# Kernel optimization log

Measured on AMD Instinct MI355X. Metric: run time of the kernel, lower is better.

## Reference

```python
import jax, jax.numpy as jnp
import numpy as np

N_NODES = 50000
N_EDGES = 800000
NEG_SLOPE = 0.2


def _gat_conv(h, src, dst, W, al, ar, b, res, act):
    """DGL-style GATConv. h:[N,Fin], W:[Fin,H*D], al/ar:[H,D], b:[H*D].
    res: None | [N,H,D] residual value. Returns [N,H,D]."""
    N = h.shape[0]
    H, D = al.shape
    ft = (h @ W).reshape(N, H, D)                       # projected features
    el = jnp.einsum('nhd,hd->nh', ft, al)               # [N,H]
    er = jnp.einsum('nhd,hd->nh', ft, ar)               # [N,H]
    e = jax.nn.leaky_relu(el[src] + er[dst], NEG_SLOPE) # [E,H] edge logits
    # edge softmax over incoming edges of each dst node
    emax = jax.ops.segment_max(e, dst, num_segments=N)  # [N,H]
    emax = jnp.where(jnp.isfinite(emax), emax, 0.0)     # guard empty segments
    ex = jnp.exp(e - emax[dst])                         # [E,H]
    denom = jax.ops.segment_sum(ex, dst, num_segments=N)
    a = ex / denom[dst]                                 # [E,H] attention
    rst = jax.ops.segment_sum(ft[src] * a[..., None], dst, num_segments=N)  # [N,H,D]
    if res is not None:
        rst = rst + res
    rst = rst + b.reshape(1, H, D)
    if act is not None:
        rst = act(rst)
    return rst


def setup_inputs() -> dict:
    key = jax.random.key(0)
    ks = jax.random.split(key, 16)
    s = 0.1
    return {
        'x': jax.random.normal(ks[0], (N_NODES, 128), jnp.float32),
        'edge_src': jax.random.randint(ks[1], (N_EDGES,), 0, N_NODES, jnp.int32),
        'edge_dst': jax.random.randint(ks[2], (N_EDGES,), 0, N_NODES, jnp.int32),
        'W0': jax.random.normal(ks[3], (128, 128), jnp.float32) * s,
        'al0': jax.random.normal(ks[4], (2, 64), jnp.float32) * s,
        'ar0': jax.random.normal(ks[5], (2, 64), jnp.float32) * s,
        'b0': jnp.zeros((128,), jnp.float32),
        'W1': jax.random.normal(ks[6], (128, 128), jnp.float32) * s,
        'al1': jax.random.normal(ks[7], (2, 64), jnp.float32) * s,
        'ar1': jax.random.normal(ks[8], (2, 64), jnp.float32) * s,
        'b1': jnp.zeros((128,), jnp.float32),
        'W2': jax.random.normal(ks[9], (128, 194), jnp.float32) * s,
        'al2': jax.random.normal(ks[10], (2, 97), jnp.float32) * s,
        'ar2': jax.random.normal(ks[11], (2, 97), jnp.float32) * s,
        'b2': jnp.zeros((194,), jnp.float32),
        'res_W2': jax.random.normal(ks[12], (128, 194), jnp.float32) * s,
    }


def reference(x, edge_src, edge_dst, W0, al0, ar0, b0, W1, al1, ar1, b1,
              W2, al2, ar2, b2, res_W2):
    N = x.shape[0]
    elu = jax.nn.elu
    # layer 0: no residual, ELU
    h = _gat_conv(x, edge_src, edge_dst, W0, al0, ar0, b0, None, elu)
    h = h.reshape(N, -1)                                # flatten(1) -> [N,128]
    # layer 1: identity residual (in == heads*out), ELU
    res1 = h.reshape(N, 2, 64)
    h = _gat_conv(h, edge_src, edge_dst, W1, al1, ar1, b1, res1, elu)
    h = h.reshape(N, -1)
    # output layer: linear residual, no activation, mean over heads
    res2 = (h @ res_W2).reshape(N, 2, 97)
    logits = _gat_conv(h, edge_src, edge_dst, W2, al2, ar2, b2, res2, None)
    logits = logits.mean(axis=1)                        # [N, 97]
    # original slices off the last node of each graph (single batched graph)
    return logits[: N - 1]
```

## Files before the change

kernel.cpp:

```cpp
#include <hip/hip_runtime.h>
#include <math.h>

#define NNODES 50000
#define NEDGES 800000
#define NPAD   50048

typedef unsigned int uint;
typedef unsigned short u16;
typedef __bf16 bf16x8 __attribute__((ext_vector_type(8)));
typedef float f32x4 __attribute__((ext_vector_type(4)));

__device__ __forceinline__ float lrelu(float x){ return x > 0.f ? x : 0.2f*x; }
__device__ __forceinline__ float elu_f(float x){ return x > 0.f ? x : expm1f(x); }
__device__ __forceinline__ u16 f2bf(float f){
    uint u = __float_as_uint(f);
    return (u16)((u + 0x7fffu + ((u >> 16) & 1u)) >> 16);
}
__device__ __forceinline__ float bf2f(u16 h){ return __uint_as_float(((uint)h) << 16); }
__device__ __forceinline__ float blo(uint u){ return __uint_as_float(u << 16); }
__device__ __forceinline__ float bhi(uint u){ return __uint_as_float(u & 0xffff0000u); }

__global__ void split_x(const float* __restrict__ x, u16* __restrict__ Xh, u16* __restrict__ Xl, int N)
{
    int idx = blockIdx.x * blockDim.x + threadIdx.x;
    if (idx >= NPAD * 32) return;
    int n = idx >> 5;
    float4 v = make_float4(0.f, 0.f, 0.f, 0.f);
    if (n < N) v = ((const float4*)x)[idx];
    ushort4 h, l;
    h.x = f2bf(v.x); l.x = f2bf(v.x - bf2f(h.x));
    h.y = f2bf(v.y); l.y = f2bf(v.y - bf2f(h.y));
    h.z = f2bf(v.z); l.z = f2bf(v.z - bf2f(h.z));
    h.w = f2bf(v.w); l.w = f2bf(v.w - bf2f(h.w));
    ((ushort4*)Xh)[idx] = h;
    ((ushort4*)Xl)[idx] = l;
}

__global__ void split_w_hi(const float* __restrict__ W, u16* __restrict__ Bh, int Cc, int CP)
{
    int idx = blockIdx.x * blockDim.x + threadIdx.x;
    if (idx >= CP * 128) return;
    int col = idx >> 7, k = idx & 127;
    float v = (col < Cc) ? W[k * Cc + col] : 0.f;
    Bh[idx] = f2bf(v);
}

__global__ void zero_pad2(u16* __restrict__ Hh, u16* __restrict__ Hl)
{
    int idx = blockIdx.x * blockDim.x + threadIdx.x;
    if (idx < (NPAD - NNODES) * 128) {
        Hh[(size_t)NNODES * 128 + idx] = 0;
        Hl[(size_t)NNODES * 128 + idx] = 0;
    }
}

__global__ __launch_bounds__(256, 4)
void gemm_l01(const u16* __restrict__ Ah, const u16* __restrict__ Al,
              const u16* __restrict__ Bh, u16* __restrict__ obf,
              const float* __restrict__ alv, const float* __restrict__ arv,
              float* __restrict__ el, float* __restrict__ er, int N)
{
    __shared__ u16 sB[128 * 136];
    const int bm = blockIdx.x * 64;
    const int tid = threadIdx.x, wid = tid >> 6, lane = tid & 63;
    const int lr = lane & 15, q = lane >> 4, lk8 = q << 3;

    bf16x8 aH[4], aL[4];
    {
        size_t abase = (size_t)(bm + wid*16 + lr) * 128 + lk8;
        #pragma unroll
        for (int kt = 0; kt < 4; kt++) {
            aH[kt] = *(const bf16x8*)(Ah + abase + kt*32);
            aL[kt] = *(const bf16x8*)(Al + abase + kt*32);
        }
    }
    {
        const int c = tid >> 1, seg = (tid & 1) * 64;
        const u16* g = Bh + (size_t)c * 128 + seg;
        u16* s = sB + c * 136 + seg;
        #pragma unroll
        for (int j = 0; j < 8; j++)
            *(uint4*)(s + j*8) = *(const uint4*)(g + j*8);
    }
    __syncthreads();

    f32x4 acc[8];
    #pragma unroll
    for (int i = 0; i < 8; i++) acc[i] = (f32x4){0.f,0.f,0.f,0.f};

    #pragma unroll
    for (int kt = 0; kt < 4; kt++)
        #pragma unroll
        for (int fs = 0; fs < 8; fs++) {
            bf16x8 b = *(const bf16x8*)(sB + (fs*16 + lr)*136 + kt*32 + lk8);
            acc[fs] = __builtin_amdgcn_mfma_f32_16x16x32_bf16(aH[kt], b, acc[fs], 0, 0, 0);
            acc[fs] = __builtin_amdgcn_mfma_f32_16x16x32_bf16(aL[kt], b, acc[fs], 0, 0, 0);
        }

    float el0[4] = {0,0,0,0}, el1[4] = {0,0,0,0}, er0[4] = {0,0,0,0}, er1[4] = {0,0,0,0};
    #pragma unroll
    for (int fs = 0; fs < 8; fs++) {
        const int col = fs*16 + lr;
        const float av = alv[col], gv = arv[col];
        #pragma unroll
        for (int v = 0; v < 4; v++) {
            float f = acc[fs][v];
            int row = bm + wid*16 + q*4 + v;
            if (row < N) obf[(size_t)row * 128 + col] = f2bf(f);
            if (fs < 4) { el0[v] += f * av; er0[v] += f * gv; }
            else        { el1[v] += f * av; er1[v] += f * gv; }
        }
    }
    #pragma unroll
    for (int off = 1; off < 16; off <<= 1) {
        #pragma unroll
        for (int v = 0; v < 4; v++) {
            el0[v] += __shfl_xor(el0[v], off);
            el1[v] += __shfl_xor(el1[v], off);
            er0[v] += __shfl_xor(er0[v], off);
            er1[v] += __shfl_xor(er1[v], off);
        }
    }
    if (lr == 0) {
        #pragma unroll
        for (int v = 0; v < 4; v++) {
            int row = bm + wid*16 + q*4 + v;
            if (row < N) {
                *(float2*)(el + 2*(size_t)row) = make_float2(el0[v], el1[v]);
                *(float2*)(er + 2*(size_t)row) = make_float2(er0[v], er1[v]);
            }
        }
    }
}

__global__ __launch_bounds__(256, 4)
void gemm_l2(const u16* __restrict__ Ah, const u16* __restrict__ Al,
             const u16* __restrict__ B2, const u16* __restrict__ Br,
             u16* __restrict__ obf, float* __restrict__ of32, int N)
{
    __shared__ u16 sB[128 * 136];
    const int bid = blockIdx.x;
    const int x = (bid >> 5) * 8 + (bid & 7);
    const int sel = (bid >> 3) & 3;
    if (x >= NPAD / 64) return;
    const bool second = (sel >= 2);
    const int coloff = (sel & 1) * 128;
    const u16* __restrict__ B = second ? Br : B2;

    const int bm = x * 64;
    const int tid = threadIdx.x, wid = tid >> 6, lane = tid & 63;
    const int lr = lane & 15, q = lane >> 4, lk8 = q << 3;

    bf16x8 aH[4], aL[4];
    {
        size_t abase = (size_t)(bm + wid*16 + lr) * 128 + lk8;
        #pragma unroll
        for (int kt = 0; kt < 4; kt++) {
            aH[kt] = *(const bf16x8*)(Ah + abase + kt*32);
            aL[kt] = *(const bf16x8*)(Al + abase + kt*32);
        }
    }
    {
        const int c = tid >> 1, seg = (tid & 1) * 64;
        const u16* g = B + (size_t)(coloff + c) * 128 + seg;
        u16* s = sB + c * 136 + seg;
        #pragma unroll
        for (int j = 0; j < 8; j++)
            *(uint4*)(s + j*8) = *(const uint4*)(g + j*8);
    }
    __syncthreads();

    f32x4 acc[8];
    #pragma unroll
    for (int i = 0; i < 8; i++) acc[i] = (f32x4){0.f,0.f,0.f,0.f};

    #pragma unroll
    for (int kt = 0; kt < 4; kt++)
        #pragma unroll
        for (int fs = 0; fs < 8; fs++) {
            bf16x8 b = *(const bf16x8*)(sB + (fs*16 + lr)*136 + kt*32 + lk8);
            acc[fs] = __builtin_amdgcn_mfma_f32_16x16x32_bf16(aH[kt], b, acc[fs], 0, 0, 0);
            acc[fs] = __builtin_amdgcn_mfma_f32_16x16x32_bf16(aL[kt], b, acc[fs], 0, 0, 0);
        }

    #pragma unroll
    for (int fs = 0; fs < 8; fs++) {
        const int col = coloff + fs*16 + lr;
        if (col >= 194) continue;
        #pragma unroll
        for (int v = 0; v < 4; v++) {
            int row = bm + wid*16 + q*4 + v;
            if (row < N) {
                if (second) of32[(size_t)row * 194 + col] = acc[fs][v];
                else        obf[(size_t)row * 194 + col] = f2bf(acc[fs][v]);
            }
        }
    }
}

template<int C, int D>
__global__ void compute_elr(const uint* __restrict__ ftb, const float* __restrict__ al,
                            const float* __restrict__ ar, float* __restrict__ el,
                            float* __restrict__ er, int N)
{
    int wv = threadIdx.x >> 6, lane = threadIdx.x & 63;
    int n = blockIdx.x * 4 + wv;
    if (n >= N) return;
    const uint* row = ftb + (size_t)n * (C/2);
    float l0=0.f, l1=0.f, r0=0.f, r1=0.f;
    for (int p = lane; p < C/2; p += 64) {
        uint u = row[p];
        float f0 = blo(u), f1 = bhi(u);
        int c0 = 2*p, c1 = 2*p + 1;
        float a0 = al[c0], a1 = al[c1], g0 = ar[c0], g1 = ar[c1];
        if (c0 < D) { l0 += f0*a0; r0 += f0*g0; } else { l1 += f0*a0; r1 += f0*g0; }
        if (c1 < D) { l0 += f1*a1; r0 += f1*g1; } else { l1 += f1*a1; r1 += f1*g1; }
    }
    #pragma unroll
    for (int off = 32; off; off >>= 1) {
        l0 += __shfl_down(l0, off); l1 += __shfl_down(l1, off);
        r0 += __shfl_down(r0, off); r1 += __shfl_down(r1, off);
    }
    if (lane == 0) { el[2*n] = l0; el[2*n+1] = l1; er[2*n] = r0; er[2*n+1] = r1; }
}

__global__ void hist_kernel(const int* __restrict__ dst, int* __restrict__ counts, int E)
{
    int i = blockIdx.x * blockDim.x + threadIdx.x;
    if (i < E) atomicAdd(&counts[dst[i]], 1);
}

__global__ __launch_bounds__(1024)
void scan_local(const int* __restrict__ counts, int* __restrict__ row_start,
                int* __restrict__ partials, int n)
{
    __shared__ int wsum[16];
    const int tid = threadIdx.x, lane = tid & 63, wv = tid >> 6;
    const int i0 = blockIdx.x * 4096 + tid * 4;
    int v[4];
    #pragma unroll
    for (int j = 0; j < 4; j++) { int i = i0 + j; v[j] = (i < n) ? counts[i] : 0; }
    v[1] += v[0]; v[2] += v[1]; v[3] += v[2];
    int t = v[3];
    #pragma unroll
    for (int off = 1; off < 64; off <<= 1) {
        int u = __shfl_up(t, off);
        if (lane >= off) t += u;
    }
    int texcl = t - v[3];
    if (lane == 63) wsum[wv] = t;
    __syncthreads();
    int woff = 0;
    for (int w = 0; w < 16; w++) if (w < wv) woff += wsum[w];
    #pragma unroll
    for (int j = 0; j < 4; j++) { int i = i0 + j; if (i < n) row_start[i+1] = woff + texcl + v[j]; }
    if (tid == 0) {
        int tot = 0;
        for (int w = 0; w < 16; w++) tot += wsum[w];
        partials[blockIdx.x] = tot;
    }
}

__global__ void scan_offs(int* __restrict__ partials, int nb)
{
    int lane = threadIdx.x;
    int v = (lane < nb) ? partials[lane] : 0;
    int t = v;
    #pragma unroll
    for (int off = 1; off < 64; off <<= 1) {
        int u = __shfl_up(t, off);
        if (lane >= off) t += u;
    }
    if (lane < nb) partials[lane] = t - v;
}

__global__ __launch_bounds__(1024)
void scan_add(int* __restrict__ row_start, const int* __restrict__ partials, int n)
{
    const int tid = threadIdx.x;
    const int add = partials[blockIdx.x];
    const int i0 = blockIdx.x * 4096 + tid * 4;
    #pragma unroll
    for (int j = 0; j < 4; j++) { int i = i0 + j; if (i < n) row_start[i+1] += add; }
    if (blockIdx.x == 0 && tid == 0) row_start[0] = 0;
}

__global__ void scatter_kernel(const int* __restrict__ src, const int* __restrict__ dst,
                               const int* __restrict__ row_start, int* __restrict__ cursor,
                               int* __restrict__ src_sorted, int E)
{
    int i = blockIdx.x * blockDim.x + threadIdx.x;
    if (i < E) {
        int d = dst[i];
        int p = atomicAdd(&cursor[d], 1);
        src_sorted[row_start[d] + p] = src[i];
    }
}

template<int MODE>
__global__ __launch_bounds__(256)
void gat_agg128(const uint* __restrict__ ftb, const float* __restrict__ el,
                const float* __restrict__ er, const int* __restrict__ row_start,
                const int* __restrict__ ssorted, const u16* __restrict__ Rh,
                const u16* __restrict__ Rl, const float* __restrict__ bias,
                u16* __restrict__ Hh, u16* __restrict__ Hl)
{
    __shared__ int   s_src[4][64];
    __shared__ float s_w[4][2][64];
    const int wv = threadIdx.x >> 6, lane = threadIdx.x & 63;
    const int n = blockIdx.x * 4 + wv;
    const int beg = row_start[n];
    const int deg = row_start[n+1] - beg;
    const float2 ern = *(const float2*)(er + 2*(size_t)n);
    const int h = lane >> 5;
    float ax = 0.f, ay = 0.f, dp0 = 0.f, dp1 = 0.f;

    for (int cb = 0; cb < deg; cb += 64) {
        const int cnt = min(64, deg - cb);
        float w0 = 0.f, w1 = 0.f; int s = 0;
        if (lane < cnt) {
            s = ssorted[beg + cb + lane];
            float2 e = *(const float2*)(el + 2*(size_t)s);
            w0 = __expf(lrelu(e.x + ern.x));
            w1 = __expf(lrelu(e.y + ern.y));
        }
        dp0 += w0; dp1 += w1;
        s_src[wv][lane] = s; s_w[wv][0][lane] = w0; s_w[wv][1][lane] = w1;
        asm volatile("s_waitcnt lgkmcnt(0)" ::: "memory");
        int t = 0;
        for (; t + 4 <= cnt; t += 4) {
            int4   s4 = *(const int4*)&s_src[wv][t];
            float4 w4 = *(const float4*)&s_w[wv][h][t];
            uint u0 = ftb[((uint)s4.x << 6) + lane];
            uint u1 = ftb[((uint)s4.y << 6) + lane];
            uint u2 = ftb[((uint)s4.z << 6) + lane];
            uint u3 = ftb[((uint)s4.w << 6) + lane];
            ax += w4.x*blo(u0); ay += w4.x*bhi(u0);
            ax += w4.y*blo(u1); ay += w4.y*bhi(u1);
            ax += w4.z*blo(u2); ay += w4.z*bhi(u2);
            ax += w4.w*blo(u3); ay += w4.w*bhi(u3);
        }
        for (; t < cnt; t++) {
            int sv = s_src[wv][t];
            float w = s_w[wv][h][t];
            uint u = ftb[((uint)sv << 6) + lane];
            ax += w*blo(u); ay += w*bhi(u);
        }
    }
    #pragma unroll
    for (int off = 32; off; off >>= 1) { dp0 += __shfl_xor(dp0, off); dp1 += __shfl_xor(dp1, off); }
    const float den = (h == 0) ? dp0 : dp1;
    float r0 = (deg > 0) ? ax / den : 0.f;
    float r1 = (deg > 0) ? ay / den : 0.f;
    const int c0 = 2 * lane;
    const size_t ob = (size_t)n*128 + c0;
    const float2 bv = *(const float2*)(bias + c0);
    float v0 = r0 + bv.x, v1 = r1 + bv.y;
    if (MODE == 1) {
        ushort2 rh = *(const ushort2*)&Rh[ob];
        ushort2 rl = *(const ushort2*)&Rl[ob];
        v0 += bf2f(rh.x) + bf2f(rl.x);
        v1 += bf2f(rh.y) + bf2f(rl.y);
    }
    v0 = elu_f(v0); v1 = elu_f(v1);
    u16 h0 = f2bf(v0), h1v = f2bf(v1);
    *(ushort2*)&Hh[ob] = make_ushort2(h0, h1v);
    *(ushort2*)&Hl[ob] = make_ushort2(f2bf(v0 - bf2f(h0)), f2bf(v1 - bf2f(h1v)));
}

__global__ __launch_bounds__(256)
void gat_agg_out(const uint* __restrict__ ftb, const float* __restrict__ el,
                 const float* __restrict__ er, const int* __restrict__ row_start,
                 const int* __restrict__ ssorted, const float* __restrict__ res,
                 const float* __restrict__ bias, float* __restrict__ out)
{
    __shared__ int   s_src[4][64];
    __shared__ float s_w[4][2][64];
    __shared__ float s_a1[4][97];
    const int wv = threadIdx.x >> 6, lane = threadIdx.x & 63;
    const int n = blockIdx.x * 4 + wv;
    if (n >= NNODES - 1) return;
    const int beg = row_start[n];
    const int deg = row_start[n+1] - beg;
    const float2 ern = *(const float2*)(er + 2*(size_t)n);
    const bool dual = (lane < 33);
    const bool xh0 = (lane <= 48), yh0 = (lane <= 47);
    float ax1=0.f, ay1=0.f, ax2=0.f, ay2=0.f, dp0=0.f, dp1=0.f;

    for (int cb = 0; cb < deg; cb += 64) {
        const int cnt = min(64, deg - cb);
        float w0 = 0.f, w1 = 0.f; int s = 0;
        if (lane < cnt) {
            s = ssorted[beg + cb + lane];
            float2 e = *(const float2*)(el + 2*(size_t)s);
            w0 = __expf(lrelu(e.x + ern.x));
            w1 = __expf(lrelu(e.y + ern.y));
        }
        dp0 += w0; dp1 += w1;
        s_src[wv][lane] = s; s_w[wv][0][lane] = w0; s_w[wv][1][lane] = w1;
        asm volatile("s_waitcnt lgkmcnt(0)" ::: "memory");
        int t = 0;
        for (; t + 4 <= cnt; t += 4) {
            int4   s4 = *(const int4*)&s_src[wv][t];
            float4 q0 = *(const float4*)&s_w[wv][0][t];
            float4 q1 = *(const float4*)&s_w[wv][1][t];
            #pragma unroll
            for (int j = 0; j < 4; j++) {
                int sv = (j==0) ? s4.x : (j==1) ? s4.y : (j==2) ? s4.z : s4.w;
                float f0 = (j==0) ? q0.x : (j==1) ? q0.y : (j==2) ? q0.z : q0.w;
                float f1 = (j==0) ? q1.x : (j==1) ? q1.y : (j==2) ? q1.z : q1.w;
                const uint* row = ftb + (uint)sv * 97u;
                uint u1 = row[lane];
                uint u2 = dual ? row[64 + lane] : 0u;
                float wx = xh0 ? f0 : f1, wy = yh0 ? f0 : f1;
                ax1 += wx*blo(u1); ay1 += wy*bhi(u1);
                ax2 += f1*blo(u2); ay2 += f1*bhi(u2);
            }
        }
        for (; t < cnt; t++) {
            int sv = s_src[wv][t];
            float f0 = s_w[wv][0][t], f1 = s_w[wv][1][t];
            const uint* row = ftb + (uint)sv * 97u;
            uint u1 = row[lane];
            uint u2 = dual ? row[64 + lane] : 0u;
            float wx = xh0 ? f0 : f1, wy = yh0 ? f0 : f1;
            ax1 += wx*blo(u1); ay1 += wy*bhi(u1);
            ax2 += f1*blo(u2); ay2 += f1*bhi(u2);
        }
    }
    #pragma unroll
    for (int off = 32; off; off >>= 1) { dp0 += __shfl_xor(dp0, off); dp1 += __shfl_xor(dp1, off); }
    const float i0 = (deg > 0) ? 1.f/dp0 : 0.f;
    const float i1 = (deg > 0) ? 1.f/dp1 : 0.f;
    float A0x = ax1 * (xh0 ? i0 : i1);
    float A0y = ay1 * (yh0 ? i0 : i1);
    float A2x = ax2 * i1, A2y = ay2 * i1;
    if (lane == 48)      s_a1[wv][0] = A0y;
    else if (lane >= 49) { s_a1[wv][2*lane - 97] = A0x; s_a1[wv][2*lane - 96] = A0y; }
    if (dual)            { s_a1[wv][31 + 2*lane] = A2x; s_a1[wv][32 + 2*lane] = A2y; }
    asm volatile("s_waitcnt lgkmcnt(0)" ::: "memory");
    if (lane <= 48) {
        const int c = 2 * lane;
        const float* rr = res + (size_t)n * 194;
        out[(size_t)n*97 + c] = 0.5f*(A0x + s_a1[wv][c] + rr[c] + rr[97+c] + bias[c] + bias[97+c]);
        if (lane < 48)
            out[(size_t)n*97 + c + 1] = 0.5f*(A0y + s_a1[wv][c+1] + rr[c+1] + rr[98+c] + bias[c+1] + bias[98+c]);
    }
}

extern "C" void kernel_launch(void* const* d_in, const int* in_sizes, int n_in,
                              void* d_out, int out_size, void* d_ws, size_t ws_size,
                              hipStream_t stream)
{
    const float* x   = (const float*)d_in[0];
    const int*   esrc= (const int*)  d_in[1];
    const int*   edst= (const int*)  d_in[2];
    const float* W0  = (const float*)d_in[3];
    const float* al0 = (const float*)d_in[4];
    const float* ar0 = (const float*)d_in[5];
    const float* b0  = (const float*)d_in[6];
    const float* W1  = (const float*)d_in[7];
    const float* al1 = (const float*)d_in[8];
    const float* ar1 = (const float*)d_in[9];
    const float* b1  = (const float*)d_in[10];
    const float* W2  = (const float*)d_in[11];
    const float* al2 = (const float*)d_in[12];
    const float* ar2 = (const float*)d_in[13];
    const float* b2  = (const float*)d_in[14];
    const float* rW2 = (const float*)d_in[15];
    float* out = (float*)d_out;

    const int N = NNODES, E = NEDGES;
    const int NB = (N + 4095) / 4096;
    float* ws = (float*)d_ws;
    size_t o = 0;
    auto alloc_f = [&](size_t count) { float* p = ws + o; o += (count + 3) & ~(size_t)3; return p; };
    float* rs2 = alloc_f((size_t)N * 194);
    float* el  = alloc_f((size_t)N * 2);
    float* er  = alloc_f((size_t)N * 2);
    uint*  ftb = (uint*)alloc_f((size_t)N * 97);
    u16* Xh  = (u16*)alloc_f((size_t)NPAD * 64);
    u16* Xl  = (u16*)alloc_f((size_t)NPAD * 64);
    u16* H1h = (u16*)alloc_f((size_t)NPAD * 64);
    u16* H1l = (u16*)alloc_f((size_t)NPAD * 64);
    u16* B0h = (u16*)alloc_f(128*64);
    u16* B1h = (u16*)alloc_f(128*64);
    u16* B2h = (u16*)alloc_f(256*64);
    u16* Brh = (u16*)alloc_f(256*64);
    int* row_start = (int*)alloc_f(N + 4);
    int* cursor    = (int*)alloc_f(N);
    int* partials  = (int*)alloc_f(64);
    int* ssorted   = (int*)alloc_f(E);

    hipMemsetAsync(cursor, 0, N * sizeof(int), stream);
    hist_kernel<<<(E + 255) / 256, 256, 0, stream>>>(edst, cursor, E);
    scan_local<<<NB, 1024, 0, stream>>>(cursor, row_start, partials, N);
    scan_offs<<<1, 64, 0, stream>>>(partials, NB);
    scan_add<<<NB, 1024, 0, stream>>>(row_start, partials, N);
    hipMemsetAsync(cursor, 0, N * sizeof(int), stream);
    scatter_kernel<<<(E + 255) / 256, 256, 0, stream>>>(esrc, edst, row_start, cursor, ssorted, E);

    split_x<<<NPAD * 32 / 256, 256, 0, stream>>>(x, Xh, Xl, N);
    split_w_hi<<<(128*128 + 255)/256, 256, 0, stream>>>(W0,  B0h, 128, 128);
    split_w_hi<<<(128*128 + 255)/256, 256, 0, stream>>>(W1,  B1h, 128, 128);
    split_w_hi<<<(256*128 + 255)/256, 256, 0, stream>>>(W2,  B2h, 194, 256);
    split_w_hi<<<(256*128 + 255)/256, 256, 0, stream>>>(rW2, Brh, 194, 256);
    zero_pad2<<<24, 256, 0, stream>>>(H1h, H1l);

    const int gx = NPAD / 64;
    const int agg_grid = N / 4;
    const int elr_grid = (N + 3) / 4;

    gemm_l01<<<gx, 256, 0, stream>>>(Xh, Xl, B0h, (u16*)ftb, al0, ar0, el, er, N);
    gat_agg128<0><<<agg_grid, 256, 0, stream>>>(ftb, el, er, row_start, ssorted, nullptr, nullptr, b0, H1h, H1l);

    gemm_l01<<<gx, 256, 0, stream>>>(H1h, H1l, B1h, (u16*)ftb, al1, ar1, el, er, N);
    gat_agg128<1><<<agg_grid, 256, 0, stream>>>(ftb, el, er, row_start, ssorted, H1h, H1l, b1, Xh, Xl);

    gemm_l2<<<((gx + 7) / 8) * 32, 256, 0, stream>>>(Xh, Xl, B2h, Brh, (u16*)ftb, rs2, N);
    compute_elr<194,97><<<elr_grid, 256, 0, stream>>>(ftb, al2, ar2, el, er, N);
    gat_agg_out<<<agg_grid, 256, 0, stream>>>(ftb, el, er, row_start, ssorted, rs2, b2, out);
}
```

Measured before the change: 330.3 us.

## Drop bf16 hi/lo split to single bf16, fuse prep kernels, unroll gathers by 8

Result: faster. 310.4 us (-6.0%).

```diff
diff --git a/kernel.cpp b/kernel.cpp
--- a/kernel.cpp
+++ b/kernel.cpp
@@ -20,43 +20,39 @@
 __device__ __forceinline__ float blo(uint u){ return __uint_as_float(u << 16); }
 __device__ __forceinline__ float bhi(uint u){ return __uint_as_float(u & 0xffff0000u); }
 
-__global__ void split_x(const float* __restrict__ x, u16* __restrict__ Xh, u16* __restrict__ Xl, int N)
+__global__ void split_x_bf(const float* __restrict__ x, u16* __restrict__ Xb,
+                           u16* __restrict__ H1b, int N)
 {
     int idx = blockIdx.x * blockDim.x + threadIdx.x;
     if (idx >= NPAD * 32) return;
     int n = idx >> 5;
-    float4 v = make_float4(0.f, 0.f, 0.f, 0.f);
-    if (n < N) v = ((const float4*)x)[idx];
-    ushort4 h, l;
-    h.x = f2bf(v.x); l.x = f2bf(v.x - bf2f(h.x));
-    h.y = f2bf(v.y); l.y = f2bf(v.y - bf2f(h.y));
-    h.z = f2bf(v.z); l.z = f2bf(v.z - bf2f(h.z));
-    h.w = f2bf(v.w); l.w = f2bf(v.w - bf2f(h.w));
-    ((ushort4*)Xh)[idx] = h;
-    ((ushort4*)Xl)[idx] = l;
-}
-
-__global__ void split_w_hi(const float* __restrict__ W, u16* __restrict__ Bh, int Cc, int CP)
+    ushort4 hv = make_ushort4(0,0,0,0);
+    if (n < N) {
+        float4 v = ((const float4*)x)[idx];
+        hv.x = f2bf(v.x); hv.y = f2bf(v.y); hv.z = f2bf(v.z); hv.w = f2bf(v.w);
+    } else {
+        ((ushort4*)H1b)[idx] = make_ushort4(0,0,0,0);
+    }
+    ((ushort4*)Xb)[idx] = hv;
+}
+
+__global__ void split_w_all(const float* __restrict__ W0, const float* __restrict__ W1,
+                            const float* __restrict__ W2, const float* __restrict__ Wr,
+                            u16* __restrict__ Ball)
 {
     int idx = blockIdx.x * blockDim.x + threadIdx.x;
-    if (idx >= CP * 128) return;
-    int col = idx >> 7, k = idx & 127;
-    float v = (col < Cc) ? W[k * Cc + col] : 0.f;
-    Bh[idx] = f2bf(v);
-}
-
-__global__ void zero_pad2(u16* __restrict__ Hh, u16* __restrict__ Hl)
-{
-    int idx = blockIdx.x * blockDim.x + threadIdx.x;
-    if (idx < (NPAD - NNODES) * 128) {
-        Hh[(size_t)NNODES * 128 + idx] = 0;
-        Hl[(size_t)NNODES * 128 + idx] = 0;
-    }
+    if (idx >= 768 * 128) return;
+    int gcol = idx >> 7, k = idx & 127;
+    float v;
+    if (gcol < 128)      v = W0[k * 128 + gcol];
+    else if (gcol < 256) v = W1[k * 128 + (gcol - 128)];
+    else if (gcol < 512) { int c = gcol - 256; v = (c < 194) ? W2[k * 194 + c] : 0.f; }
+    else                 { int c = gcol - 512; v = (c < 194) ? Wr[k * 194 + c] : 0.f; }
+    Ball[idx] = f2bf(v);
 }
 
 __global__ __launch_bounds__(256, 4)
-void gemm_l01(const u16* __restrict__ Ah, const u16* __restrict__ Al,
-              const u16* __restrict__ Bh, u16* __restrict__ obf,
+void gemm_l01(const u16* __restrict__ Ab, const u16* __restrict__ Bh, u16* __restrict__ obf,
               const float* __restrict__ alv, const float* __restrict__ arv,
               float* __restrict__ el, float* __restrict__ er, int N)
 {
@@ -65,14 +61,12 @@
     const int tid = threadIdx.x, wid = tid >> 6, lane = tid & 63;
     const int lr = lane & 15, q = lane >> 4, lk8 = q << 3;
 
-    bf16x8 aH[4], aL[4];
+    bf16x8 aH[4];
     {
         size_t abase = (size_t)(bm + wid*16 + lr) * 128 + lk8;
         #pragma unroll
-        for (int kt = 0; kt < 4; kt++) {
-            aH[kt] = *(const bf16x8*)(Ah + abase + kt*32);
-            aL[kt] = *(const bf16x8*)(Al + abase + kt*32);
-        }
+        for (int kt = 0; kt < 4; kt++)
+            aH[kt] = *(const bf16x8*)(Ab + abase + kt*32);
     }
     {
         const int c = tid >> 1, seg = (tid & 1) * 64;
@@ -94,7 +88,6 @@
         for (int fs = 0; fs < 8; fs++) {
             bf16x8 b = *(const bf16x8*)(sB + (fs*16 + lr)*136 + kt*32 + lk8);
             acc[fs] = __builtin_amdgcn_mfma_f32_16x16x32_bf16(aH[kt], b, acc[fs], 0, 0, 0);
-            acc[fs] = __builtin_amdgcn_mfma_f32_16x16x32_bf16(aL[kt], b, acc[fs], 0, 0, 0);
         }
 
     float el0[4] = {0,0,0,0}, el1[4] = {0,0,0,0}, er0[4] = {0,0,0,0}, er1[4] = {0,0,0,0};
@@ -134,9 +127,8 @@
 }
 
 __global__ __launch_bounds__(256, 4)
-void gemm_l2(const u16* __restrict__ Ah, const u16* __restrict__ Al,
-             const u16* __restrict__ B2, const u16* __restrict__ Br,
-             u16* __restrict__ obf, float* __restrict__ of32, int N)
+void gemm_l2(const u16* __restrict__ Ab, const u16* __restrict__ B2, const u16* __restrict__ Br,
+             u16* __restrict__ obf, u16* __restrict__ rs2b, int N)
 {
     __shared__ u16 sB[128 * 136];
     const int bid = blockIdx.x;
@@ -146,19 +138,18 @@
     const bool second = (sel >= 2);
     const int coloff = (sel & 1) * 128;
     const u16* __restrict__ B = second ? Br : B2;
+    u16* __restrict__ dst = second ? rs2b : obf;
 
     const int bm = x * 64;
     const int tid = threadIdx.x, wid = tid >> 6, lane = tid & 63;
     const int lr = lane & 15, q = lane >> 4, lk8 = q << 3;
 
-    bf16x8 aH[4], aL[4];
+    bf16x8 aH[4];
     {
         size_t abase = (size_t)(bm + wid*16 + lr) * 128 + lk8;
         #pragma unroll
-        for (int kt = 0; kt < 4; kt++) {
-            aH[kt] = *(const bf16x8*)(Ah + abase + kt*32);
-            aL[kt] = *(const bf16x8*)(Al + abase + kt*32);
-        }
+        for (int kt = 0; kt < 4; kt++)
+            aH[kt] = *(const bf16x8*)(Ab + abase + kt*32);
     }
     {
         const int c = tid >> 1, seg = (tid & 1) * 64;
@@ -180,7 +171,6 @@
         for (int fs = 0; fs < 8; fs++) {
             bf16x8 b = *(const bf16x8*)(sB + (fs*16 + lr)*136 + kt*32 + lk8);
             acc[fs] = __builtin_amdgcn_mfma_f32_16x16x32_bf16(aH[kt], b, acc[fs], 0, 0, 0);
-            acc[fs] = __builtin_amdgcn_mfma_f32_16x16x32_bf16(aL[kt], b, acc[fs], 0, 0, 0);
         }
 
     #pragma unroll
@@ -190,10 +180,7 @@
         #pragma unroll
         for (int v = 0; v < 4; v++) {
             int row = bm + wid*16 + q*4 + v;
-            if (row < N) {
-                if (second) of32[(size_t)row * 194 + col] = acc[fs][v];
-                else        obf[(size_t)row * 194 + col] = f2bf(acc[fs][v]);
-            }
+            if (row < N) dst[(size_t)row * 194 + col] = f2bf(acc[fs][v]);
         }
     }
 }
@@ -301,9 +288,8 @@
 __global__ __launch_bounds__(256)
 void gat_agg128(const uint* __restrict__ ftb, const float* __restrict__ el,
                 const float* __restrict__ er, const int* __restrict__ row_start,
-                const int* __restrict__ ssorted, const u16* __restrict__ Rh,
-                const u16* __restrict__ Rl, const float* __restrict__ bias,
-                u16* __restrict__ Hh, u16* __restrict__ Hl)
+                const int* __restrict__ ssorted, const u16* __restrict__ Rb,
+                const float* __restrict__ bias, u16* __restrict__ Hb)
 {
     __shared__ int   s_src[4][64];
     __shared__ float s_w[4][2][64];
@@ -328,17 +314,29 @@
         s_src[wv][lane] = s; s_w[wv][0][lane] = w0; s_w[wv][1][lane] = w1;
         asm volatile("s_waitcnt lgkmcnt(0)" ::: "memory");
         int t = 0;
+        for (; t + 8 <= cnt; t += 8) {
+            int4   sa = *(const int4*)&s_src[wv][t];
+            int4   sb = *(const int4*)&s_src[wv][t+4];
+            float4 wa = *(const float4*)&s_w[wv][h][t];
+            float4 wb = *(const float4*)&s_w[wv][h][t+4];
+            int   sv[8] = {sa.x,sa.y,sa.z,sa.w,sb.x,sb.y,sb.z,sb.w};
+            float wj[8] = {wa.x,wa.y,wa.z,wa.w,wb.x,wb.y,wb.z,wb.w};
+            uint U[8];
+            #pragma unroll
+            for (int j = 0; j < 8; j++) U[j] = ftb[((uint)sv[j] << 6) + lane];
+            #pragma unroll
+            for (int j = 0; j < 8; j++) { ax += wj[j]*blo(U[j]); ay += wj[j]*bhi(U[j]); }
+        }
         for (; t + 4 <= cnt; t += 4) {
             int4   s4 = *(const int4*)&s_src[wv][t];
             float4 w4 = *(const float4*)&s_w[wv][h][t];
-            uint u0 = ftb[((uint)s4.x << 6) + lane];
-            uint u1 = ftb[((uint)s4.y << 6) + lane];
-            uint u2 = ftb[((uint)s4.z << 6) + lane];
-            uint u3 = ftb[((uint)s4.w << 6) + lane];
-            ax += w4.x*blo(u0); ay += w4.x*bhi(u0);
-            ax += w4.y*blo(u1); ay += w4.y*bhi(u1);
-            ax += w4.z*blo(u2); ay += w4.z*bhi(u2);
-            ax += w4.w*blo(u3); ay += w4.w*bhi(u3);
+            int   sv[4] = {s4.x,s4.y,s4.z,s4.w};
+            float wj[4] = {w4.x,w4.y,w4.z,w4.w};
+            uint U[4];
+            #pragma unroll
+            for (int j = 0; j < 4; j++) U[j] = ftb[((uint)sv[j] << 6) + lane];
+            #pragma unroll
+            for (int j = 0; j < 4; j++) { ax += wj[j]*blo(U[j]); ay += wj[j]*bhi(U[j]); }
         }
         for (; t < cnt; t++) {
             int sv = s_src[wv][t];
@@ -357,21 +355,18 @@
     const float2 bv = *(const float2*)(bias + c0);
     float v0 = r0 + bv.x, v1 = r1 + bv.y;
     if (MODE == 1) {
-        ushort2 rh = *(const ushort2*)&Rh[ob];
-        ushort2 rl = *(const ushort2*)&Rl[ob];
-        v0 += bf2f(rh.x) + bf2f(rl.x);
-        v1 += bf2f(rh.y) + bf2f(rl.y);
+        ushort2 rv = *(const ushort2*)&Rb[ob];
+        v0 += bf2f(rv.x);
+        v1 += bf2f(rv.y);
     }
     v0 = elu_f(v0); v1 = elu_f(v1);
-    u16 h0 = f2bf(v0), h1v = f2bf(v1);
-    *(ushort2*)&Hh[ob] = make_ushort2(h0, h1v);
-    *(ushort2*)&Hl[ob] = make_ushort2(f2bf(v0 - bf2f(h0)), f2bf(v1 - bf2f(h1v)));
+    *(ushort2*)&Hb[ob] = make_ushort2(f2bf(v0), f2bf(v1));
 }
 
 __global__ __launch_bounds__(256)
 void gat_agg_out(const uint* __restrict__ ftb, const float* __restrict__ el,
                  const float* __restrict__ er, const int* __restrict__ row_start,
-                 const int* __restrict__ ssorted, const float* __restrict__ res,
+                 const int* __restrict__ ssorted, const u16* __restrict__ resb,
                  const float* __restrict__ bias, float* __restrict__ out)
 {
     __shared__ int   s_src[4][64];
@@ -400,21 +395,28 @@
         s_src[wv][lane] = s; s_w[wv][0][lane] = w0; s_w[wv][1][lane] = w1;
         asm volatile("s_waitcnt lgkmcnt(0)" ::: "memory");
         int t = 0;
-        for (; t + 4 <= cnt; t += 4) {
-            int4   s4 = *(const int4*)&s_src[wv][t];
-            float4 q0 = *(const float4*)&s_w[wv][0][t];
-            float4 q1 = *(const float4*)&s_w[wv][1][t];
+        for (; t + 8 <= cnt; t += 8) {
+            int4   sa = *(const int4*)&s_src[wv][t];
+            int4   sb = *(const int4*)&s_src[wv][t+4];
+            float4 p0a = *(const float4*)&s_w[wv][0][t];
+            float4 p0b = *(const float4*)&s_w[wv][0][t+4];
+            float4 p1a = *(const float4*)&s_w[wv][1][t];
+            float4 p1b = *(const float4*)&s_w[wv][1][t+4];
+            int   sv[8] = {sa.x,sa.y,sa.z,sa.w,sb.x,sb.y,sb.z,sb.w};
+            float f0[8] = {p0a.x,p0a.y,p0a.z,p0a.w,p0b.x,p0b.y,p0b.z,p0b.w};
+            float f1[8] = {p1a.x,p1a.y,p1a.z,p1a.w,p1b.x,p1b.y,p1b.z,p1b.w};
+            uint U1[8], U2[8];
             #pragma unroll
-            for (int j = 0; j < 4; j++) {
-                int sv = (j==0) ? s4.x : (j==1) ? s4.y : (j==2) ? s4.z : s4.w;
-                float f0 = (j==0) ? q0.x : (j==1) ? q0.y : (j==2) ? q0.z : q0.w;
-                float f1 = (j==0) ? q1.x : (j==1) ? q1.y : (j==2) ? q1.z : q1.w;
-                const uint* row = ftb + (uint)sv * 97u;
-                uint u1 = row[lane];
-                uint u2 = dual ? row[64 + lane] : 0u;
-                float wx = xh0 ? f0 : f1, wy = yh0 ? f0 : f1;
-                ax1 += wx*blo(u1); ay1 += wy*bhi(u1);
-                ax2 += f1*blo(u2); ay2 += f1*bhi(u2);
+            for (int j = 0; j < 8; j++) {
+                const uint* row = ftb + (uint)sv[j] * 97u;
+                U1[j] = row[lane];
+                U2[j] = dual ? row[64 + lane] : 0u;
+            }
+            #pragma unroll
+            for (int j = 0; j < 8; j++) {
+                float wx = xh0 ? f0[j] : f1[j], wy = yh0 ? f0[j] : f1[j];
+                ax1 += wx*blo(U1[j]); ay1 += wy*bhi(U1[j]);
+                ax2 += f1[j]*blo(U2[j]); ay2 += f1[j]*bhi(U2[j]);
             }
         }
         for (; t < cnt; t++) {
@@ -441,10 +443,10 @@
     asm volatile("s_waitcnt lgkmcnt(0)" ::: "memory");
     if (lane <= 48) {
         const int c = 2 * lane;
-        const float* rr = res + (size_t)n * 194;
-        out[(size_t)n*97 + c] = 0.5f*(A0x + s_a1[wv][c] + rr[c] + rr[97+c] + bias[c] + bias[97+c]);
+        const u16* rr = resb + (size_t)n * 194;
+        out[(size_t)n*97 + c] = 0.5f*(A0x + s_a1[wv][c] + bf2f(rr[c]) + bf2f(rr[97+c]) + bias[c] + bias[97+c]);
         if (lane < 48)
-            out[(size_t)n*97 + c + 1] = 0.5f*(A0y + s_a1[wv][c+1] + rr[c+1] + rr[98+c] + bias[c+1] + bias[98+c]);
+            out[(size_t)n*97 + c + 1] = 0.5f*(A0y + s_a1[wv][c+1] + bf2f(rr[c+1]) + bf2f(rr[98+c]) + bias[c+1] + bias[98+c]);
     }
 }
 
@@ -475,22 +477,18 @@
     float* ws = (float*)d_ws;
     size_t o = 0;
     auto alloc_f = [&](size_t count) { float* p = ws + o; o += (count + 3) & ~(size_t)3; return p; };
-    float* rs2 = alloc_f((size_t)N * 194);
-    float* el  = alloc_f((size_t)N * 2);
-    float* er  = alloc_f((size_t)N * 2);
-    uint*  ftb = (uint*)alloc_f((size_t)N * 97);
-    u16* Xh  = (u16*)alloc_f((size_t)NPAD * 64);
-    u16* Xl  = (u16*)alloc_f((size_t)NPAD * 64);
-    u16* H1h = (u16*)alloc_f((size_t)NPAD * 64);
-    u16* H1l = (u16*)alloc_f((size_t)NPAD * 64);
-    u16* B0h = (u16*)alloc_f(128*64);
-    u16* B1h = (u16*)alloc_f(128*64);
-    u16* B2h = (u16*)alloc_f(256*64);
-    u16* Brh = (u16*)alloc_f(256*64);
+    float* el   = alloc_f((size_t)N * 2);
+    float* er   = alloc_f((size_t)N * 2);
+    uint*  ftb  = (uint*)alloc_f((size_t)N * 97);
+    u16*   rs2b = (u16*)alloc_f((size_t)N * 97);
+    u16*   Xb   = (u16*)alloc_f((size_t)NPAD * 64);
+    u16*   H1b  = (u16*)alloc_f((size_t)NPAD * 64);
+    u16*   Ball = (u16*)alloc_f(768 * 64);
     int* row_start = (int*)alloc_f(N + 4);
     int* cursor    = (int*)alloc_f(N);
     int* partials  = (int*)alloc_f(64);
     int* ssorted   = (int*)alloc_f(E);
+    u16* B0h = Ball, *B1h = Ball + 128*128, *B2h = Ball + 256*128, *Brh = Ball + 512*128;
 
     hipMemsetAsync(cursor, 0, N * sizeof(int), stream);
     hist_kernel<<<(E + 255) / 256, 256, 0, stream>>>(edst, cursor, E);
@@ -500,24 +498,20 @@
     hipMemsetAsync(cursor, 0, N * sizeof(int), stream);
     scatter_kernel<<<(E + 255) / 256, 256, 0, stream>>>(esrc, edst, row_start, cursor, ssorted, E);
 
-    split_x<<<NPAD * 32 / 256, 256, 0, stream>>>(x, Xh, Xl, N);
-    split_w_hi<<<(128*128 + 255)/256, 256, 0, stream>>>(W0,  B0h, 128, 128);
-    split_w_hi<<<(128*128 + 255)/256, 256, 0, stream>>>(W1,  B1h, 128, 128);
-    split_w_hi<<<(256*128 + 255)/256, 256, 0, stream>>>(W2,  B2h, 194, 256);
-    split_w_hi<<<(256*128 + 255)/256, 256, 0, stream>>>(rW2, Brh, 194, 256);
-    zero_pad2<<<24, 256, 0, stream>>>(H1h, H1l);
+    split_x_bf<<<NPAD * 32 / 256, 256, 0, stream>>>(x, Xb, H1b, N);
+    split_w_all<<<768 * 128 / 256, 256, 0, stream>>>(W0, W1, W2, rW2, Ball);
 
     const int gx = NPAD / 64;
     const int agg_grid = N / 4;
     const int elr_grid = (N + 3) / 4;
 
-    gemm_l01<<<gx, 256, 0, stream>>>(Xh, Xl, B0h, (u16*)ftb, al0, ar0, el, er, N);
-    gat_agg128<0><<<agg_grid, 256, 0, stream>>>(ftb, el, er, row_start, ssorted, nullptr, nullptr, b0, H1h, H1l);
-
-    gemm_l01<<<gx, 256, 0, stream>>>(H1h, H1l, B1h, (u16*)ftb, al1, ar1, el, er, N);
-    gat_agg128<1><<<agg_grid, 256, 0, stream>>>(ftb, el, er, row_start, ssorted, H1h, H1l, b1, Xh, Xl);
-
-    gemm_l2<<<((gx + 7) / 8) * 32, 256, 0, stream>>>(Xh, Xl, B2h, Brh, (u16*)ftb, rs2, N);
+    gemm_l01<<<gx, 256, 0, stream>>>(Xb, B0h, (u16*)ftb, al0, ar0, el, er, N);
+    gat_agg128<0><<<agg_grid, 256, 0, stream>>>(ftb, el, er, row_start, ssorted, nullptr, b0, H1b);
+
+    gemm_l01<<<gx, 256, 0, stream>>>(H1b, B1h, (u16*)ftb, al1, ar1, el, er, N);
+    gat_agg128<1><<<agg_grid, 256, 0, stream>>>(ftb, el, er, row_start, ssorted, H1b, b1, Xb);
+
+    gemm_l2<<<((gx + 7) / 8) * 32, 256, 0, stream>>>(Xb, B2h, Brh, (u16*)ftb, rs2b, N);
     compute_elr<194,97><<<elr_grid, 256, 0, stream>>>(ftb, al2, ar2, el, er, N);
-    gat_agg_out<<<agg_grid, 256, 0, stream>>>(ftb, el, er, row_start, ssorted, rs2, b2, out);
-}
+    gat_agg_out<<<agg_grid, 256, 0, stream>>>(ftb, el, er, row_start, ssorted, rs2b, b2, out);
+}
```
